# Kernel optimization log

Measured on AMD Instinct MI355X. Metric: run time of the kernel, lower is better.

## Reference

```python
import jax, jax.numpy as jnp
import numpy as np

N_NODES = 100000

def gcn_conv(x, edge_index, W, b):
    # PyG GCNConv: y = D^{-1/2} (A + I) D^{-1/2} X W + b
    N = x.shape[0]
    xw = x @ W  # transform first (smaller feature dim for message passing)
    loop = jnp.arange(N, dtype=edge_index.dtype)
    src = jnp.concatenate([edge_index[0], loop])
    dst = jnp.concatenate([edge_index[1], loop])
    ones = jnp.ones(dst.shape[0], dtype=xw.dtype)
    deg = jax.ops.segment_sum(ones, dst, num_segments=N)
    dinv = jnp.where(deg > 0, jax.lax.rsqrt(deg), 0.0)
    norm = dinv[src] * dinv[dst]  # [E+N]
    msg = xw[src] * norm[:, None]  # gather + scale
    out = jax.ops.segment_sum(msg, dst, num_segments=N)  # scatter-add
    return out + b

def setup_inputs() -> dict:
    key = jax.random.key(0)
    k1, k2, k3, k4, k5 = jax.random.split(key, 5)
    num_features, hidden, num_classes = 500, 64, 40
    x = jax.random.normal(k1, (N_NODES, num_features), dtype=jnp.float32)
    edge_index = jax.random.randint(k2, (2, 1600000), 0, N_NODES, dtype=jnp.int64)
    # Glorot-style init for GCNConv weights, zero bias (PyG default)
    W1 = jax.random.normal(k3, (num_features, hidden), dtype=jnp.float32) / np.sqrt(num_features)
    b1 = jnp.zeros((hidden,), dtype=jnp.float32)
    W2 = jax.random.normal(k4, (hidden, num_classes), dtype=jnp.float32) / np.sqrt(hidden)
    b2 = jnp.zeros((num_classes,), dtype=jnp.float32)
    return {"x": x, "edge_index": edge_index, "W1": W1, "b1": b1, "W2": W2, "b2": b2}

def reference(x, edge_index, W1, b1, W2, b2):
    h = gcn_conv(x, edge_index, W1, b1)
    h = jax.nn.relu(h)
    # dropout is identity in eval mode (training=False)
    logits = gcn_conv(h, edge_index, W2, b2)
    return (jax.nn.log_softmax(logits, axis=1), logits)
```

## Files before the change

kernel.cpp:

```cpp
#include <hip/hip_runtime.h>
#include <hip/hip_bf16.h>
#include <math.h>

#define N_NODES 100000
#define F_IN    500
#define HID     64
#define NCLS    40
#define NBKT    ((N_NODES + 255) / 256)
#define STAGE_CAP 8192

typedef __attribute__((ext_vector_type(8))) short short8v;
typedef __attribute__((ext_vector_type(4))) float floatx4;
typedef unsigned short ushort_t;
typedef unsigned int uint_t;

__device__ __forceinline__ float bflo(uint_t u) {
    union { uint_t i; float f; } v; v.i = u << 16; return v.f;
}
__device__ __forceinline__ float bfhi(uint_t u) {
    union { uint_t i; float f; } v; v.i = u & 0xffff0000u; return v.f;
}
__device__ __forceinline__ ushort_t f2bf(float f) {
    __hip_bfloat16 b = __float2bfloat16(f);
    return *(ushort_t*)&b;
}


__global__ __launch_bounds__(256) void a1_count_kernel(const int* __restrict__ dst,
                                                       int* __restrict__ bcount, int E) {
    __shared__ int c[NBKT];
    for (int i = threadIdx.x; i < NBKT; i += 256) c[i] = 0;
    __syncthreads();
    int chunk = (E + gridDim.x - 1) / gridDim.x;
    int lo = blockIdx.x * chunk;
    int hi = min(lo + chunk, E);
    for (int e = lo + threadIdx.x; e < hi; e += 256) atomicAdd(&c[dst[e] >> 8], 1);
    __syncthreads();
    for (int i = threadIdx.x; i < NBKT; i += 256)
        if (c[i]) atomicAdd(&bcount[i], c[i]);
}

__global__ void scan_buckets_kernel(const int* __restrict__ bcount,
                                    int* __restrict__ boff, int* __restrict__ bcursor, int E) {
    __shared__ int s[512];
    int tid = threadIdx.x;
    int v = (tid < NBKT) ? bcount[tid] : 0;
    s[tid] = v;
    __syncthreads();
    for (int off = 1; off < 512; off <<= 1) {
        int t = (tid >= off) ? s[tid - off] : 0;
        __syncthreads();
        s[tid] += t;
        __syncthreads();
    }
    if (tid < NBKT) {
        int ex = s[tid] - v;
        boff[tid] = ex;
        bcursor[tid] = ex;
    }
    if (tid == 0) boff[NBKT] = E;
}

__global__ __launch_bounds__(256) void a2_fill_kernel(const int* __restrict__ src,
                                                      const int* __restrict__ dst,
                                                      int* __restrict__ bcursor,
                                                      int* __restrict__ pairs, int E) {
    __shared__ int c[NBKT];
    __shared__ int base[NBKT];
    for (int i = threadIdx.x; i < NBKT; i += 256) c[i] = 0;
    __syncthreads();
    int chunk = (E + gridDim.x - 1) / gridDim.x;
    int lo = blockIdx.x * chunk;
    int hi = min(lo + chunk, E);
    for (int e = lo + threadIdx.x; e < hi; e += 256) atomicAdd(&c[dst[e] >> 8], 1);
    __syncthreads();
    for (int i = threadIdx.x; i < NBKT; i += 256) {
        int nn = c[i];
        base[i] = nn ? atomicAdd(&bcursor[i], nn) : 0;
    }
    __syncthreads();
    for (int i = threadIdx.x; i < NBKT; i += 256) c[i] = 0;
    __syncthreads();
    for (int e = lo + threadIdx.x; e < hi; e += 256) {
        int d = dst[e];
        int b = d >> 8;
        int p = base[b] + atomicAdd(&c[b], 1);
        pairs[p] = src[e] | ((d & 255) << 17);
    }
}

__global__ __launch_bounds__(256) void b_fine_kernel(const int* __restrict__ pairs,
                                                     const int* __restrict__ boff,
                                                     int* __restrict__ row_ptr,
                                                     int* __restrict__ col,
                                                     float* __restrict__ dinv, int n, int E) {
    __shared__ int w[STAGE_CAP];
    __shared__ int cnt[256];
    __shared__ int scn[256];
    __shared__ int cur[256];
    int b = blockIdx.x;
    int nb0 = b << 8;
    int nodes = min(256, n - nb0);
    int g0 = boff[b], g1 = boff[b + 1];
    int size = g1 - g0;
    int stage = min(size, STAGE_CAP);
    int tid = threadIdx.x;

    for (int i = tid; i < stage; i += 256) w[i] = pairs[g0 + i];
    cnt[tid] = 0;
    __syncthreads();
    for (int i = tid; i < size; i += 256) {
        int word = (i < stage) ? w[i] : pairs[g0 + i];
        atomicAdd(&cnt[word >> 17], 1);
    }
    __syncthreads();
    int v = cnt[tid];
    scn[tid] = v;
    __syncthreads();
    for (int off = 1; off < 256; off <<= 1) {
        int t = (tid >= off) ? scn[tid - off] : 0;
        __syncthreads();
        scn[tid] += t;
        __syncthreads();
    }
    int excl = scn[tid] - v;
    cur[tid] = g0 + excl;
    if (tid < nodes) {
        row_ptr[nb0 + tid] = g0 + excl;
        dinv[nb0 + tid] = rsqrtf((float)(v + 1));
    }
    if (tid == 0 && nb0 + nodes == n) row_ptr[n] = E;
    __syncthreads();
    for (int i = tid; i < size; i += 256) {
        int word = (i < stage) ? w[i] : pairs[g0 + i];
        int pos = atomicAdd(&cur[word >> 17], 1);
        col[pos] = word & 0x1FFFF;
    }
}

__global__ void prep_w1t_kernel(const float* __restrict__ W1, ushort_t* __restrict__ W1T) {
    int idx = blockIdx.x * 256 + threadIdx.x;
    if (idx >= HID * 512) return;
    int nn = idx >> 9;
    int k  = idx & 511;
    float v = (k < F_IN) ? W1[(size_t)k * HID + nn] : 0.0f;
    W1T[idx] = f2bf(v);
}

__global__ void prep_w2t_kernel(const float* __restrict__ W2, ushort_t* __restrict__ W2bt) {
    int idx = blockIdx.x * 256 + threadIdx.x;
    if (idx >= 48 * HID) return;
    int nc = idx >> 6;
    int k  = idx & 63;
    float v = (nc < NCLS) ? W2[(size_t)k * NCLS + nc] : 0.0f;
    W2bt[idx] = f2bf(v);
}

__global__ __launch_bounds__(256) void gemm1_mfma(const float* __restrict__ x,
                                                  const ushort_t* __restrict__ W1T,
                                                  const float* __restrict__ dinv,
                                                  ushort_t* __restrict__ xws, int n) {
    __shared__ __align__(16) ushort_t As[128 * 72];
    const int tid  = threadIdx.x;
    const int wave = tid >> 6;
    const int lane = tid & 63;
    const int m16  = lane & 15;
    const int q    = lane >> 4;
    const int r0   = blockIdx.x * 128;

    floatx4 acc[2][4];
#pragma unroll
    for (int i = 0; i < 2; i++)
#pragma unroll
        for (int j = 0; j < 4; j++) acc[i][j] = (floatx4){0.f, 0.f, 0.f, 0.f};

    const int kg    = tid & 15;
    const int rbase = tid >> 4;

    for (int kb = 0; kb < 512; kb += 64) {
        __syncthreads();
        const int k4 = kb + kg * 4;
        const bool kok = (k4 < F_IN);
#pragma unroll
        for (int rr = 0; rr < 8; rr++) {
            int row = rbase + rr * 16;
            int gr  = r0 + row;
            float4 v = make_float4(0.f, 0.f, 0.f, 0.f);
            if (kok && gr < n) v = *(const float4*)&x[(size_t)gr * F_IN + k4];
            ushort_t* p = &As[row * 72 + kg * 4];
            p[0] = f2bf(v.x); p[1] = f2bf(v.y); p[2] = f2bf(v.z); p[3] = f2bf(v.w);
        }
        __syncthreads();
#pragma unroll
        for (int kt = 0; kt < 2; kt++) {
            const int ko = kt * 32 + q * 8;
            short8v a0 = *(const short8v*)&As[(wave * 32 + m16) * 72 + ko];
            short8v a1 = *(const short8v*)&As[(wave * 32 + 16 + m16) * 72 + ko];
#pragma unroll
            for (int nt = 0; nt < 4; nt++) {
                short8v b = *(const short8v*)&W1T[(size_t)(nt * 16 + m16) * 512 + kb + ko];
                acc[0][nt] = __builtin_amdgcn_mfma_f32_16x16x32_bf16(a0, b, acc[0][nt], 0, 0, 0);
                acc[1][nt] = __builtin_amdgcn_mfma_f32_16x16x32_bf16(a1, b, acc[1][nt], 0, 0, 0);
            }
        }
    }
#pragma unroll
    for (int mt = 0; mt < 2; mt++) {
#pragma unroll
        for (int i = 0; i < 4; i++) {
            int gr = r0 + wave * 32 + mt * 16 + q * 4 + i;
            if (gr < n) {
                float di = dinv[gr];
#pragma unroll
                for (int nt = 0; nt < 4; nt++) {
                    xws[(size_t)gr * HID + nt * 16 + m16] = f2bf(acc[mt][nt][i] * di);
                }
            }
        }
    }
}

__global__ __launch_bounds__(256) void agg1_kernel(const ushort_t* __restrict__ xws,
                                                   const int* __restrict__ col,
                                                   const int* __restrict__ row_ptr,
                                                   const float* __restrict__ dinv,
                                                   const float* __restrict__ b1,
                                                   ushort_t* __restrict__ h, int n) {
    int d = blockIdx.x * 4 + (threadIdx.x >> 6);
    if (d >= n) return;
    int lane = threadIdx.x & 63;
    int g = lane >> 4, c = lane & 15;
    int start = row_ptr[d], end = row_ptr[d + 1];
    uint2 selfv = *(const uint2*)&xws[(size_t)d * HID + c * 4];
    float4 acc = make_float4(0.f, 0.f, 0.f, 0.f);
    for (int j = start; j < end; j += 16) {
#pragma unroll
        for (int t = 0; t < 4; t++) {
            int e = j + t * 4 + g;
            if (e < end) {
                int s = col[e];
                uint2 v = *(const uint2*)&xws[(size_t)s * HID + c * 4];
                acc.x += bflo(v.x); acc.y += bfhi(v.x);
                acc.z += bflo(v.y); acc.w += bfhi(v.y);
            }
        }
    }
#pragma unroll
    for (int off = 16; off <= 32; off <<= 1) {
        acc.x += __shfl_xor(acc.x, off);
        acc.y += __shfl_xor(acc.y, off);
        acc.z += __shfl_xor(acc.z, off);
        acc.w += __shfl_xor(acc.w, off);
    }
    acc.x += bflo(selfv.x); acc.y += bfhi(selfv.x);
    acc.z += bflo(selfv.y); acc.w += bfhi(selfv.y);
    if (g == 0) {
        float di = dinv[d];
        float4 b = *(const float4*)&b1[c * 4];
        uint_t p0 = (uint_t)f2bf(fmaxf(di * acc.x + b.x, 0.f)) |
                    ((uint_t)f2bf(fmaxf(di * acc.y + b.y, 0.f)) << 16);
        uint_t p1 = (uint_t)f2bf(fmaxf(di * acc.z + b.z, 0.f)) |
                    ((uint_t)f2bf(fmaxf(di * acc.w + b.w, 0.f)) << 16);
        *(uint2*)&h[(size_t)d * HID + c * 4] = make_uint2(p0, p1);
    }
}

__global__ __launch_bounds__(256) void gemm2_mfma(const ushort_t* __restrict__ h,
                                                  const ushort_t* __restrict__ W2bt,
                                                  const float* __restrict__ dinv,
                                                  ushort_t* __restrict__ hws, int n) {
    int wave = threadIdx.x >> 6, lane = threadIdx.x & 63;
    int m16 = lane & 15, q = lane >> 4;
    int r0 = (blockIdx.x * 4 + wave) * 16;
    if (r0 >= n) return;
    floatx4 acc[3];
#pragma unroll
    for (int nt = 0; nt < 3; nt++) acc[nt] = (floatx4){0.f, 0.f, 0.f, 0.f};
#pragma unroll
    for (int kt = 0; kt < 2; kt++) {
        short8v a = *(const short8v*)&h[(size_t)(r0 + m16) * HID + kt * 32 + q * 8];
#pragma unroll
        for (int nt = 0; nt < 3; nt++) {
            short8v b = *(const short8v*)&W2bt[(size_t)(nt * 16 + m16) * HID + kt * 32 + q * 8];
            acc[nt] = __builtin_amdgcn_mfma_f32_16x16x32_bf16(a, b, acc[nt], 0, 0, 0);
        }
    }
#pragma unroll
    for (int i = 0; i < 4; i++) {
        int gr = r0 + q * 4 + i;
        float di = dinv[gr];
#pragma unroll
        for (int nt = 0; nt < 3; nt++) {
            int cc = nt * 16 + m16;
            hws[(size_t)gr * HID + cc] = (cc < NCLS) ? f2bf(acc[nt][i] * di) : (ushort_t)0;
        }
        hws[(size_t)gr * HID + 48 + m16] = 0;
    }
}

__global__ __launch_bounds__(256) void agg2_lsm_kernel(const ushort_t* __restrict__ hws,
                                                       const int* __restrict__ col,
                                                       const int* __restrict__ row_ptr,
                                                       const float* __restrict__ dinv,
                                                       const float* __restrict__ b2,
                                                       float* __restrict__ out, int n) {
    int d = blockIdx.x * 4 + (threadIdx.x >> 6);
    if (d >= n) return;
    int lane = threadIdx.x & 63;
    int g = lane >> 4, c = lane & 15;
    int start = row_ptr[d], end = row_ptr[d + 1];
    uint2 selfv = *(const uint2*)&hws[(size_t)d * HID + c * 4];
    float4 acc = make_float4(0.f, 0.f, 0.f, 0.f);
    for (int j = start; j < end; j += 16) {
#pragma unroll
        for (int t = 0; t < 4; t++) {
            int e = j + t * 4 + g;
            if (e < end) {
                int s = col[e];
                uint2 v = *(const uint2*)&hws[(size_t)s * HID + c * 4];
                acc.x += bflo(v.x); acc.y += bfhi(v.x);
                acc.z += bflo(v.y); acc.w += bfhi(v.y);
            }
        }
    }
#pragma unroll
    for (int off = 16; off <= 32; off <<= 1) {
        acc.x += __shfl_xor(acc.x, off);
        acc.y += __shfl_xor(acc.y, off);
        acc.z += __shfl_xor(acc.z, off);
        acc.w += __shfl_xor(acc.w, off);
    }
    acc.x += bflo(selfv.x); acc.y += bfhi(selfv.x);
    acc.z += bflo(selfv.y); acc.w += bfhi(selfv.y);

    float di = dinv[d];
    bool act = (c < 10);
    float4 b = make_float4(0.f, 0.f, 0.f, 0.f);
    if (act) b = *(const float4*)&b2[c * 4];
    float4 v;
    v.x = di * acc.x + b.x;
    v.y = di * acc.y + b.y;
    v.z = di * acc.z + b.z;
    v.w = di * acc.w + b.w;

    float m4 = act ? fmaxf(fmaxf(v.x, v.y), fmaxf(v.z, v.w)) : -INFINITY;
#pragma unroll
    for (int off = 1; off < 16; off <<= 1) m4 = fmaxf(m4, __shfl_xor(m4, off));
    float s4 = act ? (__expf(v.x - m4) + __expf(v.y - m4) + __expf(v.z - m4) + __expf(v.w - m4)) : 0.f;
#pragma unroll
    for (int off = 1; off < 16; off <<= 1) s4 += __shfl_xor(s4, off);

    if (act && g == 0) {
        float lg = __logf(s4);
        float* lsm    = out;
        float* logits = out + (size_t)N_NODES * NCLS;
        *(float4*)&logits[(size_t)d * NCLS + c * 4] = v;
        float4 o;
        o.x = v.x - m4 - lg; o.y = v.y - m4 - lg;
        o.z = v.z - m4 - lg; o.w = v.w - m4 - lg;
        *(float4*)&lsm[(size_t)d * NCLS + c * 4] = o;
    }
}

extern "C" void kernel_launch(void* const* d_in, const int* in_sizes, int n_in,
                              void* d_out, int out_size, void* d_ws, size_t ws_size,
                              hipStream_t stream) {
    const float* x  = (const float*)d_in[0];
    const int*   ei = (const int*)d_in[1];
    const float* W1 = (const float*)d_in[2];
    const float* b1 = (const float*)d_in[3];
    const float* W2 = (const float*)d_in[4];
    const float* b2 = (const float*)d_in[5];

    const int N = N_NODES;
    const int E = in_sizes[1] / 2;
    const int* src = ei;
    const int* dst = ei + E;

    ushort_t* xws  = (ushort_t*)d_ws;
    ushort_t* h    = xws + (size_t)N * HID;
    ushort_t* hws  = h + (size_t)N * HID;
    ushort_t* W1T  = hws + (size_t)N * HID;
    ushort_t* W2bt = W1T + (size_t)HID * 512;
    float* dinv    = (float*)(W2bt + 48 * HID);
    int*   row_ptr = (int*)(dinv + N);
    int*   bcount  = row_ptr + (N + 1);
    int*   boff    = bcount + 512;
    int*   bcursor = boff + 512;
    int*   pairs   = bcursor + 512;
    int*   col     = pairs + E;

    const int NB_W = (N + 3) / 4;

    hipMemsetAsync(bcount, 0, 512 * sizeof(int), stream);
    prep_w1t_kernel<<<(HID * 512 + 255) / 256, 256, 0, stream>>>(W1, W1T);
    prep_w2t_kernel<<<(48 * HID + 255) / 256, 256, 0, stream>>>(W2, W2bt);

    a1_count_kernel<<<256, 256, 0, stream>>>(dst, bcount, E);
    scan_buckets_kernel<<<1, 512, 0, stream>>>(bcount, boff, bcursor, E);
    a2_fill_kernel<<<256, 256, 0, stream>>>(src, dst, bcursor, pairs, E);
    b_fine_kernel<<<NBKT, 256, 0, stream>>>(pairs, boff, row_ptr, col, dinv, N, E);

    gemm1_mfma<<<(N + 127) / 128, 256, 0, stream>>>(x, W1T, dinv, xws, N);

    agg1_kernel<<<NB_W, 256, 0, stream>>>(xws, col, row_ptr, dinv, b1, h, N);

    gemm2_mfma<<<(N / 16 + 3) / 4, 256, 0, stream>>>(h, W2bt, dinv, hws, N);

    agg2_lsm_kernel<<<NB_W, 256, 0, stream>>>(hws, col, row_ptr, dinv, b2, (float*)d_out, N);
}
```

Measured before the change: 531.3 us.

## Double-buffer gemm1 LDS tiles with register prefetch and widen aggregation unroll

```diff
diff --git a/kernel.cpp b/kernel.cpp
--- a/kernel.cpp
+++ b/kernel.cpp
@@ -23,6 +23,9 @@
 __device__ __forceinline__ ushort_t f2bf(float f) {
     __hip_bfloat16 b = __float2bfloat16(f);
     return *(ushort_t*)&b;
+}
+__device__ __forceinline__ uint_t pack2(float a, float b) {
+    return (uint_t)f2bf(a) | ((uint_t)f2bf(b) << 16);
 }
 
 
@@ -160,7 +163,7 @@
                                                   const ushort_t* __restrict__ W1T,
                                                   const float* __restrict__ dinv,
                                                   ushort_t* __restrict__ xws, int n) {
-    __shared__ __align__(16) ushort_t As[128 * 72];
+    __shared__ __align__(16) ushort_t As[2][128 * 72];
     const int tid  = threadIdx.x;
     const int wave = tid >> 6;
     const int lane = tid & 63;
@@ -177,25 +180,44 @@
     const int kg    = tid & 15;
     const int rbase = tid >> 4;
 
-    for (int kb = 0; kb < 512; kb += 64) {
-        __syncthreads();
-        const int k4 = kb + kg * 4;
-        const bool kok = (k4 < F_IN);
+    floatx4 pf[8];
+    const floatx4 zero4 = (floatx4){0.f, 0.f, 0.f, 0.f};
+    {
+        const int k4 = kg * 4;
+#pragma unroll
+        for (int rr = 0; rr < 8; rr++) {
+            int gr = r0 + rbase + rr * 16;
+            pf[rr] = (gr < n) ? __builtin_nontemporal_load((const floatx4*)&x[(size_t)gr * F_IN + k4])
+                              : zero4;
+        }
 #pragma unroll
         for (int rr = 0; rr < 8; rr++) {
             int row = rbase + rr * 16;
-            int gr  = r0 + row;
-            float4 v = make_float4(0.f, 0.f, 0.f, 0.f);
-            if (kok && gr < n) v = *(const float4*)&x[(size_t)gr * F_IN + k4];
-            ushort_t* p = &As[row * 72 + kg * 4];
-            p[0] = f2bf(v.x); p[1] = f2bf(v.y); p[2] = f2bf(v.z); p[3] = f2bf(v.w);
-        }
-        __syncthreads();
+            *(uint2*)&As[0][row * 72 + kg * 4] =
+                make_uint2(pack2(pf[rr][0], pf[rr][1]), pack2(pf[rr][2], pf[rr][3]));
+        }
+    }
+    __syncthreads();
+
+    for (int it = 0; it < 8; it++) {
+        const int cur = it & 1;
+        if (it < 7) {
+            const int k4 = (it + 1) * 64 + kg * 4;
+            const bool kok = (k4 < F_IN);
+#pragma unroll
+            for (int rr = 0; rr < 8; rr++) {
+                int gr = r0 + rbase + rr * 16;
+                pf[rr] = (kok && gr < n)
+                           ? __builtin_nontemporal_load((const floatx4*)&x[(size_t)gr * F_IN + k4])
+                           : zero4;
+            }
+        }
+        const int kb = it * 64;
 #pragma unroll
         for (int kt = 0; kt < 2; kt++) {
             const int ko = kt * 32 + q * 8;
-            short8v a0 = *(const short8v*)&As[(wave * 32 + m16) * 72 + ko];
-            short8v a1 = *(const short8v*)&As[(wave * 32 + 16 + m16) * 72 + ko];
+            short8v a0 = *(const short8v*)&As[cur][(wave * 32 + m16) * 72 + ko];
+            short8v a1 = *(const short8v*)&As[cur][(wave * 32 + 16 + m16) * 72 + ko];
 #pragma unroll
             for (int nt = 0; nt < 4; nt++) {
                 short8v b = *(const short8v*)&W1T[(size_t)(nt * 16 + m16) * 512 + kb + ko];
@@ -203,7 +225,17 @@
                 acc[1][nt] = __builtin_amdgcn_mfma_f32_16x16x32_bf16(a1, b, acc[1][nt], 0, 0, 0);
             }
         }
-    }
+        if (it < 7) {
+#pragma unroll
+            for (int rr = 0; rr < 8; rr++) {
+                int row = rbase + rr * 16;
+                *(uint2*)&As[1 - cur][row * 72 + kg * 4] =
+                    make_uint2(pack2(pf[rr][0], pf[rr][1]), pack2(pf[rr][2], pf[rr][3]));
+            }
+            __syncthreads();
+        }
+    }
+
 #pragma unroll
     for (int mt = 0; mt < 2; mt++) {
 #pragma unroll
@@ -233,9 +265,9 @@
     int start = row_ptr[d], end = row_ptr[d + 1];
     uint2 selfv = *(const uint2*)&xws[(size_t)d * HID + c * 4];
     float4 acc = make_float4(0.f, 0.f, 0.f, 0.f);
-    for (int j = start; j < end; j += 16) {
-#pragma unroll
-        for (int t = 0; t < 4; t++) {
+    for (int j = start; j < end; j += 32) {
+#pragma unroll
+        for (int t = 0; t < 8; t++) {
             int e = j + t * 4 + g;
             if (e < end) {
                 int s = col[e];
@@ -257,10 +289,8 @@
     if (g == 0) {
         float di = dinv[d];
         float4 b = *(const float4*)&b1[c * 4];
-        uint_t p0 = (uint_t)f2bf(fmaxf(di * acc.x + b.x, 0.f)) |
-                    ((uint_t)f2bf(fmaxf(di * acc.y + b.y, 0.f)) << 16);
-        uint_t p1 = (uint_t)f2bf(fmaxf(di * acc.z + b.z, 0.f)) |
-                    ((uint_t)f2bf(fmaxf(di * acc.w + b.w, 0.f)) << 16);
+        uint_t p0 = pack2(fmaxf(di * acc.x + b.x, 0.f), fmaxf(di * acc.y + b.y, 0.f));
+        uint_t p1 = pack2(fmaxf(di * acc.z + b.z, 0.f), fmaxf(di * acc.w + b.w, 0.f));
         *(uint2*)&h[(size_t)d * HID + c * 4] = make_uint2(p0, p1);
     }
 }
@@ -311,9 +341,9 @@
     int start = row_ptr[d], end = row_ptr[d + 1];
     uint2 selfv = *(const uint2*)&hws[(size_t)d * HID + c * 4];
     float4 acc = make_float4(0.f, 0.f, 0.f, 0.f);
-    for (int j = start; j < end; j += 16) {
-#pragma unroll
-        for (int t = 0; t < 4; t++) {
+    for (int j = start; j < end; j += 32) {
+#pragma unroll
+        for (int t = 0; t < 8; t++) {
             int e = j + t * 4 + g;
             if (e < end) {
                 int s = col[e];
@@ -392,7 +422,7 @@
 
     const int NB_W = (N + 3) / 4;
 
-    hipMemsetAsync(bcount, 0, 512 * sizeof(int), stream);
+    (void)hipMemsetAsync(bcount, 0, 512 * sizeof(int), stream);
     prep_w1t_kernel<<<(HID * 512 + 255) / 256, 256, 0, stream>>>(W1, W1T);
     prep_w2t_kernel<<<(48 * HID + 255) / 256, 256, 0, stream>>>(W2, W2bt);
 
```

New measurement: 526.5 us. Within noise of the previous version (-0.9%).
